# Optimization experiments

Hardware: AMD Instinct MI355X
Metric: run time of the kernel (lower is better)

Reference implementation:

```python
import jax, jax.numpy as jnp
import numpy as np

CH = 64
INTER = 8  # max(64 // 8, 1)


def setup_inputs() -> dict:
    key = jax.random.key(0)
    ks = jax.random.split(key, 8)
    B, C, H, W = 4, CH, 64, 64
    x = jax.random.normal(ks[0], (B, C, H, W), dtype=jnp.float32)
    s = 1.0 / np.sqrt(C)
    Wq = jax.random.normal(ks[1], (INTER, C), dtype=jnp.float32) * s
    bq = jnp.zeros((INTER,), dtype=jnp.float32)
    Wk = jax.random.normal(ks[2], (INTER, C), dtype=jnp.float32) * s
    bk = jnp.zeros((INTER,), dtype=jnp.float32)
    Wv = jax.random.normal(ks[3], (C, C), dtype=jnp.float32) * s
    bv = jnp.zeros((C,), dtype=jnp.float32)
    gamma = jax.random.normal(ks[4], (1,), dtype=jnp.float32) * 0.1
    return {"x": x, "Wq": Wq, "bq": bq, "Wk": Wk, "bk": bk, "Wv": Wv, "bv": bv, "gamma": gamma}


def reference(x, Wq, bq, Wk, bk, Wv, bv, gamma):
    B, C, H, W = x.shape
    xf = x.reshape(B, C, H * W)  # [B, C, N]
    # 1x1 convs == per-pixel linear projections
    q = jnp.einsum('dc,bcn->bdn', Wq, xf) + bq[None, :, None]  # [B, d, N]
    k = jnp.einsum('dc,bcn->bdn', Wk, xf) + bk[None, :, None]  # [B, d, N]
    v = jnp.einsum('ec,bcn->ben', Wv, xf) + bv[None, :, None]  # [B, C, N]
    scale = 1.0 / np.sqrt(INTER).astype(np.float32)
    scores = jnp.einsum('bdi,bdj->bij', q, k) * scale  # [B, N, N]
    attn = jax.nn.softmax(scores, axis=-1)
    out = jnp.einsum('bcj,bij->bci', v, attn)  # value @ attn^T
    out = out.reshape(B, C, H, W)
    return gamma[0] * out + x
```

## Files before the change

kernel.cpp:

```cpp
#include <hip/hip_runtime.h>
#include <hip/hip_bf16.h>
#include <stdint.h>

#define BATCH 4
#define CCH   64
#define NPIX  4096
#define DQK   8
#define PXB   128

typedef __attribute__((ext_vector_type(8)))  short bf16x8;
typedef __attribute__((ext_vector_type(16))) float f32x16;
typedef __attribute__((ext_vector_type(4)))  uint32_t u32x4;

static __device__ __forceinline__ short f2bf(float f) {
    union { __hip_bfloat16 h; short s; } u;
    u.h = __float2bfloat16(f);
    return u.s;
}
static __device__ __forceinline__ uint32_t cvt_pk_bf16(float lo, float hi) {
    uint32_t r;
    asm("v_cvt_pk_bf16_f32 %0, %1, %2" : "=v"(r) : "v"(lo), "v"(hi));
    return r;
}

__global__ __launch_bounds__(256) void proj_kernel(
    const float* __restrict__ x,
    const float* __restrict__ Wq, const float* __restrict__ bq,
    const float* __restrict__ Wk, const float* __restrict__ bk,
    const float* __restrict__ Wv, const float* __restrict__ bv,
    short* __restrict__ qo, short* __restrict__ ko, short* __restrict__ vo)
{
    __shared__ float xs[CCH][PXB];
    __shared__ float wv_s[CCH][68];
    __shared__ float wq_s[CCH][DQK];
    __shared__ float wk_s[CCH][DQK];

    const int b  = blockIdx.x >> 5;
    const int n0 = (blockIdx.x & 31) * PXB;
    const int tid = threadIdx.x;

    for (int i = tid; i < CCH*CCH; i += 256) wv_s[i & 63][i >> 6] = Wv[i];
    for (int i = tid; i < CCH*DQK; i += 256) { wq_s[i & 63][i >> 6] = Wq[i]; wk_s[i & 63][i >> 6] = Wk[i]; }
    for (int i = tid; i < CCH*PXB; i += 256) {
        int c = i >> 7, p = i & 127;
        xs[c][p] = x[((size_t)b*CCH + c)*NPIX + n0 + p];
    }
    __syncthreads();

    const int p0 = tid & 31;
    const int g  = tid >> 5;
    const int e0 = g * 8;

    float av[4][8];
    float aq[4], ak[4];
    #pragma unroll
    for (int pi = 0; pi < 4; ++pi) {
        #pragma unroll
        for (int i = 0; i < 8; ++i) av[pi][i] = bv[e0 + i];
        aq[pi] = bq[g]; ak[pi] = bk[g];
    }

    for (int c = 0; c < CCH; ++c) {
        float4 w0 = *(const float4*)&wv_s[c][e0];
        float4 w1 = *(const float4*)&wv_s[c][e0 + 4];
        float wq = wq_s[c][g], wk = wk_s[c][g];
        #pragma unroll
        for (int pi = 0; pi < 4; ++pi) {
            float xv = xs[c][p0 + 32*pi];
            av[pi][0] += w0.x*xv; av[pi][1] += w0.y*xv;
            av[pi][2] += w0.z*xv; av[pi][3] += w0.w*xv;
            av[pi][4] += w1.x*xv; av[pi][5] += w1.y*xv;
            av[pi][6] += w1.z*xv; av[pi][7] += w1.w*xv;
            aq[pi] += wq*xv; ak[pi] += wk*xv;
        }
    }

    const float qscale = 0.51010407112635f;
    const size_t vb = (size_t)b * CCH * NPIX;
    #pragma unroll
    for (int pi = 0; pi < 4; ++pi) {
        const int px = n0 + p0 + 32*pi;
        #pragma unroll
        for (int i = 0; i < 8; ++i)
            vo[vb + (size_t)(e0 + i)*NPIX + px] = f2bf(av[pi][i]);
        const size_t qb = ((size_t)b*NPIX + px)*16 + g;
        qo[qb]     = f2bf(aq[pi] * qscale);
        qo[qb + 8] = 0;
        ko[qb]     = f2bf(ak[pi]);
        ko[qb + 8] = 0;
    }
}

__global__ __launch_bounds__(512, 4) void attn_kernel(
    const short* __restrict__ qg, const short* __restrict__ kg,
    const short* __restrict__ vg,
    const float* __restrict__ x, const float* __restrict__ gamma,
    float* __restrict__ outp)
{
    __shared__ __align__(16) char smem[32768];
    __shared__ float l_s[8][32];
    __shared__ float linv_s[32];

    char*  vs_c = smem;
    float* mbuf = (float*)smem;

    const int qt = blockIdx.x & 127;
    const int b  = blockIdx.x >> 7;
    const int i0 = qt << 5;
    const int tid  = threadIdx.x;
    const int wave = tid >> 6, lane = tid & 63;
    const int hi = lane >> 5, li = lane & 31;

    f32x16 z16;
    #pragma unroll
    for (int r = 0; r < 16; ++r) z16[r] = 0.f;

    const bf16x8 qf = *(const bf16x8*)&qg[((size_t)b*NPIX + i0 + li)*16 + hi*8];

    f32x16 acc0 = z16, acc1 = z16;
    float l_run = 0.f;

    const short* kp = kg + (size_t)b * NPIX * 16;
    const size_t vbase = (size_t)b * CCH * NPIX;

    const int sc  = tid >> 3;
    const short* vsrc = vg + vbase + (size_t)sc*NPIX + (tid & 7)*8;
    const int   wb  = (tid & 7) * 16;
    const int   swz = (sc & 15) << 4;
    char* wp = vs_c + sc*512;

    const int  rswz = (li & 15) << 4;
    const int  rb0  = (wave << 6) + (hi << 4);
    char* rp0 = vs_c + li*512;
    char* rp1 = vs_c + (li + 32)*512;

    int4 st0 = *(const int4*)(vsrc);
    int4 st1 = *(const int4*)(vsrc + 64);
    int4 st2 = *(const int4*)(vsrc + 128);
    int4 st3 = *(const int4*)(vsrc + 192);
    bf16x8 akf = *(const bf16x8*)&kp[(size_t)((wave << 5) + li)*16 + hi*8];

    for (int win = 0; win < 16; ++win) {
        *(int4*)(wp + ((wb +   0) ^ swz)) = st0;
        *(int4*)(wp + ((wb + 128) ^ swz)) = st1;
        *(int4*)(wp + ((wb + 256) ^ swz)) = st2;
        *(int4*)(wp + ((wb + 384) ^ swz)) = st3;
        if (win < 15) {
            const short* ns = vsrc + (win + 1)*256;
            st0 = *(const int4*)(ns);
            st1 = *(const int4*)(ns + 64);
            st2 = *(const int4*)(ns + 128);
            st3 = *(const int4*)(ns + 192);
        }
        __syncthreads();

        f32x16 S = __builtin_amdgcn_mfma_f32_32x32x16_bf16(akf, qf, z16, 0, 0, 0);
        if (win < 15) {
            const int jn = ((win + 1) << 8) + (wave << 5);
            akf = *(const bf16x8*)&kp[(size_t)(jn + li)*16 + hi*8];
        }

        bf16x8 av00 = *(const bf16x8*)(rp0 + ((rb0     ) ^ rswz));
        bf16x8 av01 = *(const bf16x8*)(rp0 + ((rb0 + 32) ^ rswz));
        bf16x8 av10 = *(const bf16x8*)(rp1 + ((rb0     ) ^ rswz));
        bf16x8 av11 = *(const bf16x8*)(rp1 + ((rb0 + 32) ^ rswz));

        #pragma unroll
        for (int r = 0; r < 16; ++r) S[r] = __builtin_amdgcn_exp2f(S[r]);

        {
            float s0 = (S[0]+S[1]) + (S[2]+S[3]);
            float s1 = (S[4]+S[5]) + (S[6]+S[7]);
            float s2 = (S[8]+S[9]) + (S[10]+S[11]);
            float s3 = (S[12]+S[13]) + (S[14]+S[15]);
            l_run += (s0+s1) + (s2+s3);
        }

        uint32_t a01 = cvt_pk_bf16(S[0], S[1]);
        uint32_t a23 = cvt_pk_bf16(S[2], S[3]);
        uint32_t a45 = cvt_pk_bf16(S[4], S[5]);
        uint32_t a67 = cvt_pk_bf16(S[6], S[7]);
        uint32_t a89 = cvt_pk_bf16(S[8], S[9]);
        uint32_t aab = cvt_pk_bf16(S[10], S[11]);
        uint32_t acd = cvt_pk_bf16(S[12], S[13]);
        uint32_t aef = cvt_pk_bf16(S[14], S[15]);
        asm("v_permlane32_swap_b32 %0, %1" : "+v"(a01), "+v"(a45));
        asm("v_permlane32_swap_b32 %0, %1" : "+v"(a23), "+v"(a67));
        asm("v_permlane32_swap_b32 %0, %1" : "+v"(a89), "+v"(acd));
        asm("v_permlane32_swap_b32 %0, %1" : "+v"(aab), "+v"(aef));
        u32x4 pw0 = { a01, a23, a45, a67 };
        u32x4 pw1 = { a89, aab, acd, aef };
        bf16x8 b0 = __builtin_bit_cast(bf16x8, pw0);
        bf16x8 b1 = __builtin_bit_cast(bf16x8, pw1);

        __builtin_amdgcn_s_setprio(1);
        acc0 = __builtin_amdgcn_mfma_f32_32x32x16_bf16(av00, b0, acc0, 0, 0, 0);
        acc1 = __builtin_amdgcn_mfma_f32_32x32x16_bf16(av10, b0, acc1, 0, 0, 0);
        acc0 = __builtin_amdgcn_mfma_f32_32x32x16_bf16(av01, b1, acc0, 0, 0, 0);
        acc1 = __builtin_amdgcn_mfma_f32_32x32x16_bf16(av11, b1, acc1, 0, 0, 0);
        __builtin_amdgcn_s_setprio(0);
        __syncthreads();
    }

    l_run += __shfl_xor(l_run, 32);
    if (hi == 0) l_s[wave][li] = l_run;

    if (wave < 4) {
        #pragma unroll
        for (int r = 0; r < 16; ++r) {
            int row = (r & 3) + ((r >> 2) << 3) + (hi << 2);
            mbuf[(wave*64 + row)*32 + li]      = acc0[r];
            mbuf[(wave*64 + row + 32)*32 + li] = acc1[r];
        }
    }
    __syncthreads();
    if (wave >= 4) {
        #pragma unroll
        for (int r = 0; r < 16; ++r) {
            int row = (r & 3) + ((r >> 2) << 3) + (hi << 2);
            mbuf[((wave-4)*64 + row)*32 + li]      += acc0[r];
            mbuf[((wave-4)*64 + row + 32)*32 + li] += acc1[r];
        }
    } else if (tid < 32) {
        float L = 0.f;
        #pragma unroll
        for (int w = 0; w < 8; ++w) L += l_s[w][tid];
        linv_s[tid] = __builtin_amdgcn_rcpf(L);
    }
    __syncthreads();

    const float g0 = gamma[0];
    for (int idx = tid; idx < CCH*32; idx += 512) {
        int c = idx >> 5, i = idx & 31;
        float s = mbuf[c*32 + i] + mbuf[(64 + c)*32 + i]
                + mbuf[(128 + c)*32 + i] + mbuf[(192 + c)*32 + i];
        size_t gidx = vbase + (size_t)c*NPIX + i0 + i;
        outp[gidx] = g0 * (s * linv_s[i]) + x[gidx];
    }
}

extern "C" void kernel_launch(void* const* d_in, const int* in_sizes, int n_in,
                              void* d_out, int out_size, void* d_ws, size_t ws_size,
                              hipStream_t stream) {
    const float* x     = (const float*)d_in[0];
    const float* Wq    = (const float*)d_in[1];
    const float* bq    = (const float*)d_in[2];
    const float* Wk    = (const float*)d_in[3];
    const float* bk    = (const float*)d_in[4];
    const float* Wv    = (const float*)d_in[5];
    const float* bv    = (const float*)d_in[6];
    const float* gamma = (const float*)d_in[7];

    short* qo = (short*)d_ws;
    short* ko = qo + (size_t)BATCH*NPIX*16;
    short* vo = ko + (size_t)BATCH*NPIX*16;

    proj_kernel<<<BATCH*(NPIX/PXB), 256, 0, stream>>>(x, Wq, bq, Wk, bk, Wv, bv, qo, ko, vo);
    attn_kernel<<<BATCH*(NPIX/32), 512, 0, stream>>>(qo, ko, vo, x, gamma, (float*)d_out);
}
```

Measured before the change: 101.6 us.

## Double-buffer V tiles in LDS to drop one barrier per window

Turns the single 32KB LDS staging buffer for V into two 32KB buffers that alternate each window. The next window's tile is written into the other buffer while the current one is read, with global loads issued two windows ahead, so the barrier before compute is removed. The cost is doubled LDS (64KB) and the launch-bounds occupancy hint falling from 4 to 2 blocks per CU, which can reduce latency hiding.

```diff
diff --git a/kernel.cpp b/kernel.cpp
--- a/kernel.cpp
+++ b/kernel.cpp
@@ -91,17 +91,16 @@
     }
 }
 
-__global__ __launch_bounds__(512, 4) void attn_kernel(
+__global__ __launch_bounds__(512, 2) void attn_kernel(
     const short* __restrict__ qg, const short* __restrict__ kg,
     const short* __restrict__ vg,
     const float* __restrict__ x, const float* __restrict__ gamma,
     float* __restrict__ outp)
 {
-    __shared__ __align__(16) char smem[32768];
+    __shared__ __align__(16) char smem[65536];
     __shared__ float l_s[8][32];
     __shared__ float linv_s[32];
 
-    char*  vs_c = smem;
     float* mbuf = (float*)smem;
 
     const int qt = blockIdx.x & 127;
@@ -127,32 +126,49 @@
     const short* vsrc = vg + vbase + (size_t)sc*NPIX + (tid & 7)*8;
     const int   wb  = (tid & 7) * 16;
     const int   swz = (sc & 15) << 4;
-    char* wp = vs_c + sc*512;
+    const int   wrow = sc*512;
 
     const int  rswz = (li & 15) << 4;
     const int  rb0  = (wave << 6) + (hi << 4);
-    char* rp0 = vs_c + li*512;
-    char* rp1 = vs_c + (li + 32)*512;
+    const int  rrow0 = li*512;
+    const int  rrow1 = (li + 32)*512;
 
     int4 st0 = *(const int4*)(vsrc);
     int4 st1 = *(const int4*)(vsrc + 64);
     int4 st2 = *(const int4*)(vsrc + 128);
     int4 st3 = *(const int4*)(vsrc + 192);
-    bf16x8 akf = *(const bf16x8*)&kp[(size_t)((wave << 5) + li)*16 + hi*8];
-
-    for (int win = 0; win < 16; ++win) {
+    {
+        char* wp = smem + wrow;
         *(int4*)(wp + ((wb +   0) ^ swz)) = st0;
         *(int4*)(wp + ((wb + 128) ^ swz)) = st1;
         *(int4*)(wp + ((wb + 256) ^ swz)) = st2;
         *(int4*)(wp + ((wb + 384) ^ swz)) = st3;
+    }
+    st0 = *(const int4*)(vsrc + 256);
+    st1 = *(const int4*)(vsrc + 320);
+    st2 = *(const int4*)(vsrc + 384);
+    st3 = *(const int4*)(vsrc + 448);
+    bf16x8 akf = *(const bf16x8*)&kp[(size_t)((wave << 5) + li)*16 + hi*8];
+    __syncthreads();
+
+    for (int win = 0; win < 16; ++win) {
+        char* cur = smem + ((win & 1) << 15);
+        char* nxt = smem + (((win + 1) & 1) << 15);
+
         if (win < 15) {
-            const short* ns = vsrc + (win + 1)*256;
+            char* wp = nxt + wrow;
+            *(int4*)(wp + ((wb +   0) ^ swz)) = st0;
+            *(int4*)(wp + ((wb + 128) ^ swz)) = st1;
+            *(int4*)(wp + ((wb + 256) ^ swz)) = st2;
+            *(int4*)(wp + ((wb + 384) ^ swz)) = st3;
+        }
+        if (win < 14) {
+            const short* ns = vsrc + (win + 2)*256;
             st0 = *(const int4*)(ns);
             st1 = *(const int4*)(ns + 64);
             st2 = *(const int4*)(ns + 128);
             st3 = *(const int4*)(ns + 192);
         }
-        __syncthreads();
 
         f32x16 S = __builtin_amdgcn_mfma_f32_32x32x16_bf16(akf, qf, z16, 0, 0, 0);
         if (win < 15) {
@@ -160,10 +176,10 @@
             akf = *(const bf16x8*)&kp[(size_t)(jn + li)*16 + hi*8];
         }
 
-        bf16x8 av00 = *(const bf16x8*)(rp0 + ((rb0     ) ^ rswz));
-        bf16x8 av01 = *(const bf16x8*)(rp0 + ((rb0 + 32) ^ rswz));
-        bf16x8 av10 = *(const bf16x8*)(rp1 + ((rb0     ) ^ rswz));
-        bf16x8 av11 = *(const bf16x8*)(rp1 + ((rb0 + 32) ^ rswz));
+        bf16x8 av00 = *(const bf16x8*)(cur + rrow0 + ((rb0     ) ^ rswz));
+        bf16x8 av01 = *(const bf16x8*)(cur + rrow0 + ((rb0 + 32) ^ rswz));
+        bf16x8 av10 = *(const bf16x8*)(cur + rrow1 + ((rb0     ) ^ rswz));
+        bf16x8 av11 = *(const bf16x8*)(cur + rrow1 + ((rb0 + 32) ^ rswz));
 
         #pragma unroll
         for (int r = 0; r < 16; ++r) S[r] = __builtin_amdgcn_exp2f(S[r]);
@@ -199,6 +215,7 @@
         acc0 = __builtin_amdgcn_mfma_f32_32x32x16_bf16(av01, b1, acc0, 0, 0, 0);
         acc1 = __builtin_amdgcn_mfma_f32_32x32x16_bf16(av11, b1, acc1, 0, 0, 0);
         __builtin_amdgcn_s_setprio(0);
+
         __syncthreads();
     }
 
```

Result: no change. 102.0 us (+0.4%).
